# Kernel optimization log

Hardware: AMD Instinct MI355X
Metric: run time of the kernel (lower is better)

Reference implementation:

```python
import jax, jax.numpy as jnp
from jax import lax
import numpy as np

S, WL, V, E, OC, H = 512, 100, 50000, 200, 50, 400  # sents, words, vocab, emb, conv out-ch, hidden


def setup_inputs() -> dict:
    key = jax.random.key(0)
    ks = jax.random.split(key, 40)
    lengths = jax.random.randint(ks[0], (S,), 20, WL + 1)
    tok = jax.random.randint(ks[1], (S, WL), 1, V)
    x = jnp.where(jnp.arange(WL)[None, :] < lengths[:, None], tok, 0)  # 0 = pad

    def p(i, shape):
        return jax.random.normal(ks[i], shape, jnp.float32) * 0.05

    inp = {"x": x, "num_of_sent": 3, "emb": p(2, (V, E))}
    for K in range(8):
        inp[f"conv_w{K}"] = p(3 + K, (OC, E, 2 * K + 1))
    inp["conv_b"] = p(11, (8, OC))
    names = ["w_ih_f", "w_hh_f", "b_ih_f", "b_hh_f", "w_ih_b", "w_hh_b", "b_ih_b", "b_hh_b"]
    shapes = [(3 * H, H), (3 * H, H), (3 * H,), (3 * H,)] * 2
    for j, (n, s) in enumerate(zip(names, shapes)):
        inp[n] = p(12 + j, s)
    inp["W_doc"] = p(20, (H, 2 * H)); inp["b_doc"] = p(21, (H,))
    inp["W_d1"] = p(22, (100, 4 * H)); inp["b_d1"] = p(23, (100,))
    inp["W_d2"] = p(24, (1, 100)); inp["b_d2"] = p(25, (1,))
    inp["W_r"] = p(26, (H, 2 * H)); inp["b_r"] = p(27, (H,))
    return inp


def _gru_dir(xs, w_ih, w_hh, b_ih, b_hh, reverse):
    gi = xs @ w_ih.T + b_ih  # [S, 3H] input projections precomputed

    def step(h, gi_t):
        gh = w_hh @ h + b_hh
        r = jax.nn.sigmoid(gi_t[:H] + gh[:H])
        z = jax.nn.sigmoid(gi_t[H:2 * H] + gh[H:2 * H])
        n = jnp.tanh(gi_t[2 * H:] + r * gh[2 * H:])
        h_new = (1.0 - z) * n + z * h
        return h_new, h_new

    return lax.scan(step, jnp.zeros(H, xs.dtype), gi, reverse=reverse)[1]


def _forward(x, num_of_sent, emb, conv_ws, conv_b, gru_f, gru_b,
             W_doc, b_doc, W_d1, b_d1, W_d2, b_d2, W_r, b_r):
    lengths = (x > 0).sum(axis=1)  # sum(sign(x), dim=1)
    wf = emb[x]                            # [S, WL, E]
    ci = jnp.swapaxes(wf, 1, 2)            # [S, E, WL]
    dn = ('NCH', 'OIH', 'NCH')
    feats = [lax.conv_general_dilated(ci, w, (1,), 'SAME', dimension_numbers=dn)
             + conv_b[k][None, :, None] for k, w in enumerate(conv_ws)]
    sf = jnp.swapaxes(jnp.concatenate(feats, axis=1), 1, 2)  # [S, WL, 400]
    mask = (jnp.arange(WL)[None, :] < lengths[:, None]).astype(sf.dtype)
    pooled = (sf * mask[:, :, None]).sum(axis=1) / lengths[:, None].astype(sf.dtype)  # ragged avg-pool [S,400]
    hf = _gru_dir(pooled, *gru_f, reverse=False)
    hb = _gru_dir(pooled, *gru_b, reverse=True)
    enc = jnp.concatenate([hf, hb], axis=1)  # [S, 800]
    doc = jnp.tanh(W_doc @ enc.mean(axis=0) + b_doc)  # [400]

    def dec_step(carry, enc_i):
        g, count = carry
        feat = jnp.concatenate([enc_i, g, doc])  # [1600]
        p = jax.nn.sigmoid(W_d2 @ jnp.tanh(W_d1 @ feat + b_d1) + b_d2)[0]
        allowed = jnp.logical_or(num_of_sent <= 0, count < num_of_sent)
        sel = jnp.logical_and(allowed, p > 0.5)  # greedy decision
        g = g + sel.astype(g.dtype) * jnp.tanh(W_r @ enc_i + b_r)
        count = count + sel.astype(count.dtype)
        term = jnp.where(sel, p, 1.0 - p)
        return (g, count), (term, sel)

    init = (jnp.zeros(H, enc.dtype), jnp.zeros((), jnp.int32))
    _, (terms, sels) = lax.scan(dec_step, init, enc)
    logp = jnp.log(terms * 0.99999 + 5e-6).sum()
    return logp, sels.astype(jnp.int32)


def reference(x, num_of_sent, emb, conv_w0, conv_w1, conv_w2, conv_w3, conv_w4, conv_w5, conv_w6, conv_w7,
              conv_b, w_ih_f, w_hh_f, b_ih_f, b_hh_f, w_ih_b, w_hh_b, b_ih_b, b_hh_b,
              W_doc, b_doc, W_d1, b_d1, W_d2, b_d2, W_r, b_r):
    conv_ws = (conv_w0, conv_w1, conv_w2, conv_w3, conv_w4, conv_w5, conv_w6, conv_w7)
    gru_f = (w_ih_f, w_hh_f, b_ih_f, b_hh_f)
    gru_b = (w_ih_b, w_hh_b, b_ih_b, b_hh_b)
    return _forward(x, num_of_sent, emb, conv_ws, conv_b, gru_f, gru_b,
                    W_doc, b_doc, W_d1, b_d1, W_d2, b_d2, W_r, b_r)
```

## Files before the change

kernel.cpp:

```cpp
#include <hip/hip_runtime.h>
#include <math.h>

#define S_N   512
#define WL_N  100
#define E_N   200
#define OC_N  50
#define H_N   400

__global__ __launch_bounds__(256, 1)
void window_kernel(const int* __restrict__ x, const float* __restrict__ emb,
                   float* __restrict__ Awin)
{
  const int s = blockIdx.x;
  const int tid = threadIdx.x;
  __shared__ int xr[WL_N];
  __shared__ int Lsh;
  __shared__ float Apart[E_N][17];
  __shared__ float Bpart[E_N][9];
  if (tid < WL_N) xr[tid] = x[s * WL_N + tid];
  __syncthreads();
  if (tid == 0) {
    int L = 0;
    for (int t = 0; t < WL_N; ++t) L += (xr[t] != 0) ? 1 : 0;
    Lsh = L;
  }
  __syncthreads();
  const int L = Lsh;
  const int Lp7 = (L + 7 < WL_N) ? (L + 7) : WL_N;
  if (tid < E_N) {
    const int e = tid;
    float acc = 0.f;
    for (int t = 0; t < Lp7; ++t) {
      acc += emb[(size_t)xr[t] * E_N + e];
      int m = t + 1;
      if (m <= 7) Bpart[e][m] = acc;
      int rel = m - (L - 7);
      if (rel >= 0 && rel < 15) Apart[e][rel] = acc;
    }
    const float accF = acc;
    const float invL = 1.f / (float)L;
    #pragma unroll
    for (int dd = 0; dd < 15; ++dd) {
      int m = L - 7 + dd;
      float A = (m > WL_N) ? accF : Apart[e][dd];
      int d = dd - 7;
      float B = (d > 0) ? Bpart[e][d] : 0.f;
      Awin[(size_t)s * 3000 + dd * 200 + e] = (A - B) * invL;
    }
  }
}

__global__ __launch_bounds__(256, 2)
void gemm_pool(const float* __restrict__ Awin,
               const float* __restrict__ cw0, const float* __restrict__ cw1,
               const float* __restrict__ cw2, const float* __restrict__ cw3,
               const float* __restrict__ cw4, const float* __restrict__ cw5,
               const float* __restrict__ cw6, const float* __restrict__ cw7,
               const float* __restrict__ conv_b,
               float* __restrict__ pooled)
{
  __shared__ float As[16][65];
  __shared__ float Bs[16][65];
  const int bm = blockIdx.y * 64, bn = blockIdx.x * 64;
  const int tid = threadIdx.x;
  const int tr = (tid / 16) * 4, tc = (tid % 16) * 4;
  const int c = tid & 15;

  const float* cwA[8] = {cw0, cw1, cw2, cw3, cw4, cw5, cw6, cw7};
  const float* base_i[4];
  int lo_i[4], w_i[4];
  bool valid_i[4];
  #pragma unroll
  for (int i = 0; i < 4; ++i) {
    int gcol = bn + (tid >> 4) + 16 * i;
    bool v = (gcol < 400);
    int g = v ? gcol : 0;
    int K = g / 50, oc = g % 50;
    int width = 2 * K + 1;
    valid_i[i] = v;
    lo_i[i] = 7 - K;
    w_i[i] = width;
    base_i[i] = cwA[K] + (size_t)oc * 200 * width;
  }

  float acc[4][4] = {};
  int e = c, dd = 0;
  for (int k0 = 0; k0 < 3000; k0 += 16) {
    for (int l = tid; l < 64 * 16; l += 256) {
      int r = l >> 4, cc2 = l & 15;
      int k = k0 + cc2;
      As[cc2][r] = (k < 3000) ? Awin[(size_t)(bm + r) * 3000 + k] : 0.f;
    }
    #pragma unroll
    for (int i = 0; i < 4; ++i) {
      int r = (tid >> 4) + 16 * i;
      int off = dd - lo_i[i];
      float v = 0.f;
      if (valid_i[i] && off >= 0 && off < w_i[i])
        v = base_i[i][e * w_i[i] + off];
      Bs[c][r] = v;
    }
    __syncthreads();
    #pragma unroll
    for (int kk = 0; kk < 16; ++kk) {
      float a[4], b[4];
      #pragma unroll
      for (int u = 0; u < 4; ++u) { a[u] = As[kk][tr + u]; b[u] = Bs[kk][tc + u]; }
      #pragma unroll
      for (int u = 0; u < 4; ++u)
        #pragma unroll
        for (int v = 0; v < 4; ++v) acc[u][v] += a[u] * b[v];
    }
    __syncthreads();
    e += 16;
    if (e >= 200) { e -= 200; dd += 1; }
  }
  for (int u = 0; u < 4; ++u) {
    int r = bm + tr + u;
    for (int v = 0; v < 4; ++v) {
      int cc2 = bn + tc + v; if (cc2 >= 400) continue;
      pooled[(size_t)r * 400 + cc2] = acc[u][v] + conv_b[cc2];
    }
  }
}

__global__ __launch_bounds__(256, 2)
void gemm_gi(const float* __restrict__ A,
             const float* __restrict__ wf, const float* __restrict__ bf,
             const float* __restrict__ wb, const float* __restrict__ bb,
             float* __restrict__ C,
             unsigned long long* __restrict__ hz)
{
  __shared__ float As[16][65];
  __shared__ float Bs[16][65];
  const int bm = blockIdx.y * 64, bn = blockIdx.x * 64;
  const int tid = threadIdx.x;
  const int tr = (tid / 16) * 4, tc = (tid % 16) * 4;
  if (blockIdx.x == 0 && blockIdx.y == 0)
    for (int l = tid; l < 1600; l += 256) hz[l] = 0ull;
  float acc[4][4] = {};
  for (int k0 = 0; k0 < 400; k0 += 16) {
    for (int l = tid; l < 64 * 16; l += 256) {
      int r = l / 16, c = l % 16;
      As[c][r] = A[(size_t)(bm + r) * 400 + k0 + c];
    }
    for (int l = tid; l < 64 * 16; l += 256) {
      int r = l / 16, c = l % 16;
      int gcol = bn + r;
      float v = 0.f;
      if (gcol < 1200)      v = wf[(size_t)gcol * 400 + k0 + c];
      else if (gcol < 2400) v = wb[(size_t)(gcol - 1200) * 400 + k0 + c];
      Bs[c][r] = v;
    }
    __syncthreads();
    #pragma unroll
    for (int kk = 0; kk < 16; ++kk) {
      float a[4], b[4];
      #pragma unroll
      for (int u = 0; u < 4; ++u) { a[u] = As[kk][tr + u]; b[u] = Bs[kk][tc + u]; }
      #pragma unroll
      for (int u = 0; u < 4; ++u)
        #pragma unroll
        for (int v = 0; v < 4; ++v) acc[u][v] += a[u] * b[v];
    }
    __syncthreads();
  }
  for (int u = 0; u < 4; ++u) {
    int r = bm + tr + u;
    for (int v = 0; v < 4; ++v) {
      int c = bn + tc + v; if (c >= 2400) continue;
      float bias = (c < 1200) ? bf[c] : bb[c - 1200];
      C[(size_t)r * 2400 + c] = acc[u][v] + bias;
    }
  }
}

template<int TAG>
__global__ __launch_bounds__(256, 4)
void gemm32(const float* __restrict__ A, int lda,
            const float* __restrict__ Bw, int ldb,
            const float* __restrict__ bias,
            float* __restrict__ C, int ldc,
            int M, int N, int K, int act)
{
  __shared__ float As[32][33];
  __shared__ float Bs[32][33];
  const int bm = blockIdx.y * 32, bn = blockIdx.x * 32;
  const int tid = threadIdx.x;
  const int tr = (tid >> 4) * 2, tc = (tid & 15) * 2;
  float acc[2][2] = {};
  for (int k0 = 0; k0 < K; k0 += 32) {
    #pragma unroll
    for (int p = 0; p < 4; ++p) {
      int l = tid + p * 256;
      int r = l >> 5, c = l & 31;
      As[c][r] = (bm + r < M) ? A[(size_t)(bm + r) * lda + k0 + c] : 0.f;
      Bs[c][r] = (bn + r < N) ? Bw[(size_t)(bn + r) * ldb + k0 + c] : 0.f;
    }
    __syncthreads();
    #pragma unroll
    for (int kk = 0; kk < 32; ++kk) {
      float a0 = As[kk][tr], a1 = As[kk][tr + 1];
      float b0 = Bs[kk][tc], b1 = Bs[kk][tc + 1];
      acc[0][0] += a0 * b0; acc[0][1] += a0 * b1;
      acc[1][0] += a1 * b0; acc[1][1] += a1 * b1;
    }
    __syncthreads();
  }
  #pragma unroll
  for (int u = 0; u < 2; ++u) {
    int r = bm + tr + u; if (r >= M) continue;
    #pragma unroll
    for (int v = 0; v < 2; ++v) {
      int c = bn + tc + v; if (c >= N) continue;
      float xv = acc[u][v] + (bias ? bias[c] : 0.f);
      if (act == 1) xv = tanhf(xv);
      C[(size_t)r * ldc + c] = xv;
    }
  }
}

#define GRU_NB 25
#define GRU_CHUNK 16
#define LDA64(p) __hip_atomic_load((p), __ATOMIC_RELAXED, __HIP_MEMORY_SCOPE_AGENT)
__global__ __launch_bounds__(256, 1)
void gru_scan_kernel(const float* __restrict__ gi,
                     const float* __restrict__ whh_f, const float* __restrict__ bhh_f,
                     const float* __restrict__ whh_b, const float* __restrict__ bhh_b,
                     float* __restrict__ enc,
                     float* __restrict__ mean,
                     unsigned long long* __restrict__ hbuf)
{
  const int tid = threadIdx.x;
  const int dir = blockIdx.x / GRU_NB;
  const int b   = blockIdx.x % GRU_NB;
  const float* whh = dir ? whh_b : whh_f;
  const float* bhh = dir ? bhh_b : bhh_f;
  unsigned long long* hb = hbuf + (size_t)dir * 800;
  const int i0 = b * GRU_CHUNK;

  __shared__ float wl[48][400];
  __shared__ float hs[400];
  __shared__ float ghs[48];

  for (int l = tid; l < 48 * 400; l += 256) {
    int lr = l / 400, c = l % 400;
    int g = lr / GRU_CHUNK, ii = lr % GRU_CHUNK;
    wl[lr][c] = whh[(size_t)(g * 400 + i0 + ii) * 400 + c];
  }

  const int i  = tid >> 4;
  const int cc = tid & 15;
  const int c0 = cc * 25;

  float blr = 0.f, blz = 0.f, bln = 0.f, msum = 0.f;
  float g0r = 0.f, g0z = 0.f, g0n = 0.f;
  float g1r = 0.f, g1z = 0.f, g1n = 0.f;
  if (tid < GRU_CHUNK) {
    blr = bhh[i0 + tid];
    blz = bhh[400 + i0 + tid];
    bln = bhh[800 + i0 + tid];
    {
      int t0 = dir ? 511 : 0;
      const float* g = gi + (size_t)t0 * 2400 + dir * 1200 + i0 + tid;
      g0r = g[0]; g0z = g[400]; g0n = g[800];
      int t1 = dir ? 510 : 1;
      g = gi + (size_t)t1 * 2400 + dir * 1200 + i0 + tid;
      g1r = g[0]; g1z = g[400]; g1n = g[800];
    }
  }
  __syncthreads();

  const int p = tid - 64;
  const bool h2 = (p >= 0) && (p < 16);

  for (int t = 0; t < 512; ++t) {
    const int t_in = dir ? (511 - t) : t;
    if (tid >= 64) {
      const unsigned long long* src = hb + (t & 1) * 400;
      const unsigned want = (unsigned)t;
      unsigned long long a0, a1, a2 = 0, b0, b1, b2 = 0, r0, r1, r2 = 0;
      a0 = LDA64(src + p); a1 = LDA64(src + p + 192); if (h2) a2 = LDA64(src + p + 384);
      b0 = LDA64(src + p); b1 = LDA64(src + p + 192); if (h2) b2 = LDA64(src + p + 384);
      for (;;) {
        bool ok = ((unsigned)(a0 >> 32) == want) && ((unsigned)(a1 >> 32) == want)
                  && (!h2 || ((unsigned)(a2 >> 32) == want));
        if (__all(ok)) { r0 = a0; r1 = a1; r2 = a2; break; }
        a0 = LDA64(src + p); a1 = LDA64(src + p + 192); if (h2) a2 = LDA64(src + p + 384);
        ok = ((unsigned)(b0 >> 32) == want) && ((unsigned)(b1 >> 32) == want)
             && (!h2 || ((unsigned)(b2 >> 32) == want));
        if (__all(ok)) { r0 = b0; r1 = b1; r2 = b2; break; }
        b0 = LDA64(src + p); b1 = LDA64(src + p + 192); if (h2) b2 = LDA64(src + p + 384);
      }
      hs[p] = __uint_as_float((unsigned)r0);
      hs[p + 192] = __uint_as_float((unsigned)r1);
      if (h2) hs[p + 384] = __uint_as_float((unsigned)r2);
    }
    __syncthreads();

    float a0 = 0.f, a1 = 0.f, a2 = 0.f;
    #pragma unroll
    for (int j = 0; j < 25; ++j) {
      float hv = hs[c0 + j];
      a0 += wl[i][c0 + j] * hv;
      a1 += wl[16 + i][c0 + j] * hv;
      a2 += wl[32 + i][c0 + j] * hv;
    }
    #pragma unroll
    for (int m = 1; m <= 8; m <<= 1) {
      a0 += __shfl_xor(a0, m);
      a1 += __shfl_xor(a1, m);
      a2 += __shfl_xor(a2, m);
    }
    if (cc == 0) { ghs[i] = a0; ghs[16 + i] = a1; ghs[32 + i] = a2; }
    __syncthreads();

    if (tid < GRU_CHUNK) {
      float r = 1.f / (1.f + expf(-(g0r + ghs[tid] + blr)));
      float z = 1.f / (1.f + expf(-(g0z + ghs[16 + tid] + blz)));
      float n = tanhf(g0n + r * (ghs[32 + tid] + bln));
      float hprev = hs[i0 + tid];
      float hn = (1.f - z) * n + z * hprev;
      msum += hn;
      unsigned long long pk =
          ((unsigned long long)(unsigned)(t + 1) << 32) |
          (unsigned long long)__float_as_uint(hn);
      __hip_atomic_store(hb + ((t + 1) & 1) * 400 + i0 + tid, pk,
                         __ATOMIC_RELAXED, __HIP_MEMORY_SCOPE_AGENT);
      enc[(size_t)t_in * 800 + dir * 400 + i0 + tid] = hn;
      g0r = g1r; g0z = g1z; g0n = g1n;
      int t2 = t + 2; if (t2 > 511) t2 = 511;
      int tn2 = dir ? (511 - t2) : t2;
      const float* g = gi + (size_t)tn2 * 2400 + dir * 1200 + i0 + tid;
      g1r = g[0]; g1z = g[400]; g1n = g[800];
    }
  }
  if (tid < GRU_CHUNK)
    mean[dir * 400 + i0 + tid] = msum * (1.f / 512.f);
}

__global__ __launch_bounds__(1024, 1)
void decoder_kernel(const float* __restrict__ pre1,
                    const float* __restrict__ Qb,
                    const float* __restrict__ mean,
                    const float* __restrict__ W_doc,
                    const float* __restrict__ b_doc,
                    const float* __restrict__ W_d1,
                    const float* __restrict__ W_d2,
                    const float* __restrict__ b_d2,
                    const int* __restrict__ nos_p,
                    float* __restrict__ out)
{
  const int tid = threadIdx.x;
  const int row = tid >> 1;
  const int half = tid & 1;
  __shared__ float mean_s[800];
  __shared__ float doc_s[400];
  __shared__ float dt_s[100];
  __shared__ float q[100];
  __shared__ float w2s[100];
  __shared__ int   selfl[512];
  __shared__ int   firstpos;
  __shared__ float red[16];

  if (tid < 800) mean_s[tid] = mean[tid];
  if (tid < 100) { q[tid] = 0.f; w2s[tid] = W_d2[tid]; }
  if (tid < 512) selfl[tid] = 0;
  __syncthreads();

  const int w = tid >> 6, l = tid & 63;
  for (int rr = 0; rr < 25; ++rr) {
    int r = w * 25 + rr;
    float s = 0.f;
    for (int k = l; k < 800; k += 64) s += W_doc[(size_t)r * 800 + k] * mean_s[k];
    s += __shfl_xor(s, 1);  s += __shfl_xor(s, 2);  s += __shfl_xor(s, 4);
    s += __shfl_xor(s, 8);  s += __shfl_xor(s, 16); s += __shfl_xor(s, 32);
    if (l == 0) doc_s[r] = tanhf(s + b_doc[r]);
  }
  __syncthreads();
  for (int r = w; r < 100; r += 16) {
    float s = 0.f;
    for (int k = l; k < 400; k += 64) s += W_d1[(size_t)r * 1600 + 1200 + k] * doc_s[k];
    s += __shfl_xor(s, 1);  s += __shfl_xor(s, 2);  s += __shfl_xor(s, 4);
    s += __shfl_xor(s, 8);  s += __shfl_xor(s, 16); s += __shfl_xor(s, 32);
    if (l == 0) dt_s[r] = s;
  }
  __syncthreads();

  float pr[50];
  #pragma unroll
  for (int k = 0; k < 50; ++k)
    pr[k] = pre1[(size_t)row * 100 + half * 50 + k] + dt_s[half * 50 + k];
  const float bd2 = b_d2[0];
  const int nos = nos_p[0];
  int count = 0, seg = 0;
  float logp_part = 0.f;
  __syncthreads();

  for (int pass = 0; pass < 600 && seg < 512; ++pass) {
    const bool allowed = (nos <= 0) || (count < nos);
    if (tid == 0) firstpos = 512;
    float acc = 0.f;
    #pragma unroll
    for (int k = 0; k < 50; ++k)
      acc += w2s[half * 50 + k] * tanhf(pr[k] + q[half * 50 + k]);
    acc += __shfl_xor(acc, 1);
    const float sv = acc + bd2;
    __syncthreads();
    if (allowed && half == 0 && row >= seg && sv > 0.f)
      atomicMin(&firstpos, row);
    __syncthreads();
    const int fp = allowed ? firstpos : 512;
    const int lim = (fp < 512) ? fp : 511;
    if (half == 0 && row >= seg && row <= lim) {
      float p = 1.f / (1.f + expf(-sv));
      float term = (row == fp) ? p : (1.f - p);
      logp_part += logf(term * 0.99999f + 5e-6f);
      if (row == fp) selfl[row] = 1;
    }
    if (fp < 512) {
      if (tid < 100) q[tid] += Qb[(size_t)fp * 100 + tid];
      count += 1;
      seg = fp + 1;
    } else {
      seg = 512;
    }
    __syncthreads();
  }

  float v = logp_part;
  v += __shfl_xor(v, 1);  v += __shfl_xor(v, 2);  v += __shfl_xor(v, 4);
  v += __shfl_xor(v, 8);  v += __shfl_xor(v, 16); v += __shfl_xor(v, 32);
  if ((tid & 63) == 0) red[tid >> 6] = v;
  __syncthreads();
  if (tid == 0) {
    float s = 0.f;
    #pragma unroll
    for (int ww = 0; ww < 16; ++ww) s += red[ww];
    out[0] = s;
  }
  if (half == 0) out[1 + row] = (float)selfl[row];
}

extern "C" void kernel_launch(void* const* d_in, const int* in_sizes, int n_in,
                              void* d_out, int out_size, void* d_ws, size_t ws_size,
                              hipStream_t stream) {
  const int*   x      = (const int*)  d_in[0];
  const int*   nos    = (const int*)  d_in[1];
  const float* emb    = (const float*)d_in[2];
  const float* cw[8];
  for (int k = 0; k < 8; ++k) cw[k] = (const float*)d_in[3 + k];
  const float* conv_b = (const float*)d_in[11];
  const float* w_ih_f = (const float*)d_in[12];
  const float* w_hh_f = (const float*)d_in[13];
  const float* b_ih_f = (const float*)d_in[14];
  const float* b_hh_f = (const float*)d_in[15];
  const float* w_ih_b = (const float*)d_in[16];
  const float* w_hh_b = (const float*)d_in[17];
  const float* b_ih_b = (const float*)d_in[18];
  const float* b_hh_b = (const float*)d_in[19];
  const float* W_doc  = (const float*)d_in[20];
  const float* b_doc  = (const float*)d_in[21];
  const float* W_d1   = (const float*)d_in[22];
  const float* b_d1   = (const float*)d_in[23];
  const float* W_d2   = (const float*)d_in[24];
  const float* b_d2   = (const float*)d_in[25];
  const float* W_r    = (const float*)d_in[26];
  const float* b_r    = (const float*)d_in[27];

  float* ws = (float*)d_ws;
  float* Awin   = ws;
  float* gi     = ws;
  float* Rbuf   = ws;
  float* Qbuf   = ws + 204800;
  unsigned long long* hbuf = (unsigned long long*)(ws + 1228800);
  float* pooled = ws + 1536000;
  float* pre1   = ws + 1536000;
  float* mean   = ws + 1587200;
  float* enc    = ws + 1740800;

  window_kernel<<<512, 256, 0, stream>>>(x, emb, Awin);

  gemm_pool<<<dim3(7, 8), 256, 0, stream>>>(Awin, cw[0], cw[1], cw[2], cw[3],
                                            cw[4], cw[5], cw[6], cw[7],
                                            conv_b, pooled);

  gemm_gi<<<dim3(38, 8), 256, 0, stream>>>(pooled, w_ih_f, b_ih_f, w_ih_b, b_ih_b,
                                           gi, hbuf);

  gru_scan_kernel<<<2 * GRU_NB, 256, 0, stream>>>(gi, w_hh_f, b_hh_f, w_hh_b, b_hh_b,
                                                  enc, mean, hbuf);

  gemm32<1><<<dim3(13, 16), 256, 0, stream>>>(enc, 800, W_r, 800, b_r,
                                              Rbuf, 400, 512, 400, 800, 1);
  gemm32<2><<<dim3(4, 16), 256, 0, stream>>>(Rbuf, 400, W_d1 + 800, 1600, nullptr,
                                             Qbuf, 100, 512, 100, 400, 0);
  gemm32<3><<<dim3(4, 16), 256, 0, stream>>>(enc, 800, W_d1, 1600, b_d1,
                                             pre1, 100, 512, 100, 800, 0);

  decoder_kernel<<<1, 1024, 0, stream>>>(pre1, Qbuf, mean, W_doc, b_doc, W_d1,
                                         W_d2, b_d2, nos, (float*)d_out);
}
```

Before: 1.998 ms.

## Pre-pad conv weights into a dense matrix and use generic gemm32 for pooling

```diff
diff --git a/kernel.cpp b/kernel.cpp
--- a/kernel.cpp
+++ b/kernel.cpp
@@ -9,7 +9,7 @@
 
 __global__ __launch_bounds__(256, 1)
 void window_kernel(const int* __restrict__ x, const float* __restrict__ emb,
-                   float* __restrict__ Awin)
+                   float* __restrict__ Awin, int stride)
 {
   const int s = blockIdx.x;
   const int tid = threadIdx.x;
@@ -18,6 +18,8 @@
   __shared__ float Apart[E_N][17];
   __shared__ float Bpart[E_N][9];
   if (tid < WL_N) xr[tid] = x[s * WL_N + tid];
+  for (int idx = tid; idx < stride - 3000; idx += 256)
+    Awin[(size_t)s * stride + 3000 + idx] = 0.f;
   __syncthreads();
   if (tid == 0) {
     int L = 0;
@@ -45,8 +47,33 @@
       float A = (m > WL_N) ? accF : Apart[e][dd];
       int d = dd - 7;
       float B = (d > 0) ? Bpart[e][d] : 0.f;
-      Awin[(size_t)s * 3000 + dd * 200 + e] = (A - B) * invL;
-    }
+      Awin[(size_t)s * stride + dd * 200 + e] = (A - B) * invL;
+    }
+  }
+}
+
+__global__ __launch_bounds__(256, 4)
+void pad_kernel(const float* __restrict__ cw0, const float* __restrict__ cw1,
+                const float* __restrict__ cw2, const float* __restrict__ cw3,
+                const float* __restrict__ cw4, const float* __restrict__ cw5,
+                const float* __restrict__ cw6, const float* __restrict__ cw7,
+                float* __restrict__ Wpad)
+{
+  const int gcol = blockIdx.x;
+  const int tid = threadIdx.x;
+  const float* cwA[8] = {cw0, cw1, cw2, cw3, cw4, cw5, cw6, cw7};
+  const int K = gcol / 50, oc = gcol % 50;
+  const int width = 2 * K + 1;
+  const int lo = 7 - K;
+  const float* base = cwA[K] + (size_t)oc * 200 * width;
+  for (int k = tid; k < 3072; k += 256) {
+    float v = 0.f;
+    if (k < 3000) {
+      int dd = k / 200, e = k - dd * 200;
+      int off = dd - lo;
+      if (off >= 0 && off < width) v = base[e * width + off];
+    }
+    Wpad[(size_t)gcol * 3072 + k] = v;
   }
 }
 
@@ -469,35 +496,63 @@
   const float* b_r    = (const float*)d_in[27];
 
   float* ws = (float*)d_ws;
-  float* Awin   = ws;
-  float* gi     = ws;
-  float* Rbuf   = ws;
-  float* Qbuf   = ws + 204800;
-  unsigned long long* hbuf = (unsigned long long*)(ws + 1228800);
-  float* pooled = ws + 1536000;
-  float* pre1   = ws + 1536000;
-  float* mean   = ws + 1587200;
-  float* enc    = ws + 1740800;
-
-  window_kernel<<<512, 256, 0, stream>>>(x, emb, Awin);
-
-  gemm_pool<<<dim3(7, 8), 256, 0, stream>>>(Awin, cw[0], cw[1], cw[2], cw[3],
-                                            cw[4], cw[5], cw[6], cw[7],
-                                            conv_b, pooled);
-
-  gemm_gi<<<dim3(38, 8), 256, 0, stream>>>(pooled, w_ih_f, b_ih_f, w_ih_b, b_ih_b,
-                                           gi, hbuf);
-
-  gru_scan_kernel<<<2 * GRU_NB, 256, 0, stream>>>(gi, w_hh_f, b_hh_f, w_hh_b, b_hh_b,
-                                                  enc, mean, hbuf);
-
-  gemm32<1><<<dim3(13, 16), 256, 0, stream>>>(enc, 800, W_r, 800, b_r,
-                                              Rbuf, 400, 512, 400, 800, 1);
-  gemm32<2><<<dim3(4, 16), 256, 0, stream>>>(Rbuf, 400, W_d1 + 800, 1600, nullptr,
-                                             Qbuf, 100, 512, 100, 400, 0);
-  gemm32<3><<<dim3(4, 16), 256, 0, stream>>>(enc, 800, W_d1, 1600, b_d1,
-                                             pre1, 100, 512, 100, 800, 0);
-
-  decoder_kernel<<<1, 1024, 0, stream>>>(pre1, Qbuf, mean, W_doc, b_doc, W_d1,
-                                         W_d2, b_d2, nos, (float*)d_out);
-}
+  const size_t NEED_FAST = (size_t)3009664 * 4;
+
+  if (ws_size >= NEED_FAST) {
+    float* Awin   = ws;
+    float* Wpad   = ws + 1572864;
+    float* pooled = ws + 2801664;
+    float* gi     = ws;
+    unsigned long long* hbuf = (unsigned long long*)(ws + 3006464);
+    float* enc    = ws + 1572864;
+    float* mean   = ws + 1982464;
+    float* Rbuf   = ws;
+    float* Qbuf   = ws + 204800;
+    float* pre1   = ws + 2801664;
+
+    window_kernel<<<512, 256, 0, stream>>>(x, emb, Awin, 3072);
+    pad_kernel<<<400, 256, 0, stream>>>(cw[0], cw[1], cw[2], cw[3],
+                                        cw[4], cw[5], cw[6], cw[7], Wpad);
+    gemm32<0><<<dim3(13, 16), 256, 0, stream>>>(Awin, 3072, Wpad, 3072, conv_b,
+                                                pooled, 400, 512, 400, 3072, 0);
+    gemm_gi<<<dim3(38, 8), 256, 0, stream>>>(pooled, w_ih_f, b_ih_f, w_ih_b, b_ih_b,
+                                             gi, hbuf);
+    gru_scan_kernel<<<2 * GRU_NB, 256, 0, stream>>>(gi, w_hh_f, b_hh_f, w_hh_b, b_hh_b,
+                                                    enc, mean, hbuf);
+    gemm32<1><<<dim3(13, 16), 256, 0, stream>>>(enc, 800, W_r, 800, b_r,
+                                                Rbuf, 400, 512, 400, 800, 1);
+    gemm32<2><<<dim3(4, 16), 256, 0, stream>>>(Rbuf, 400, W_d1 + 800, 1600, nullptr,
+                                               Qbuf, 100, 512, 100, 400, 0);
+    gemm32<3><<<dim3(4, 16), 256, 0, stream>>>(enc, 800, W_d1, 1600, b_d1,
+                                               pre1, 100, 512, 100, 800, 0);
+    decoder_kernel<<<1, 1024, 0, stream>>>(pre1, Qbuf, mean, W_doc, b_doc, W_d1,
+                                           W_d2, b_d2, nos, (float*)d_out);
+  } else {
+    float* Awin   = ws;
+    float* gi     = ws;
+    float* Rbuf   = ws;
+    float* Qbuf   = ws + 204800;
+    unsigned long long* hbuf = (unsigned long long*)(ws + 1228800);
+    float* pooled = ws + 1536000;
+    float* pre1   = ws + 1536000;
+    float* mean   = ws + 1587200;
+    float* enc    = ws + 1740800;
+
+    window_kernel<<<512, 256, 0, stream>>>(x, emb, Awin, 3000);
+    gemm_pool<<<dim3(7, 8), 256, 0, stream>>>(Awin, cw[0], cw[1], cw[2], cw[3],
+                                              cw[4], cw[5], cw[6], cw[7],
+                                              conv_b, pooled);
+    gemm_gi<<<dim3(38, 8), 256, 0, stream>>>(pooled, w_ih_f, b_ih_f, w_ih_b, b_ih_b,
+                                             gi, hbuf);
+    gru_scan_kernel<<<2 * GRU_NB, 256, 0, stream>>>(gi, w_hh_f, b_hh_f, w_hh_b, b_hh_b,
+                                                    enc, mean, hbuf);
+    gemm32<1><<<dim3(13, 16), 256, 0, stream>>>(enc, 800, W_r, 800, b_r,
+                                                Rbuf, 400, 512, 400, 800, 1);
+    gemm32<2><<<dim3(4, 16), 256, 0, stream>>>(Rbuf, 400, W_d1 + 800, 1600, nullptr,
+                                               Qbuf, 100, 512, 100, 400, 0);
+    gemm32<3><<<dim3(4, 16), 256, 0, stream>>>(enc, 800, W_d1, 1600, b_d1,
+                                               pre1, 100, 512, 100, 800, 0);
+    decoder_kernel<<<1, 1024, 0, stream>>>(pre1, Qbuf, mean, W_doc, b_doc, W_d1,
+                                           W_d2, b_d2, nos, (float*)d_out);
+  }
+}
```

Result: faster. 1.808 ms (-9.5%).
